# Kernel optimization log

Hardware: AMD Instinct MI355X
Metric: run time of the kernel (lower is better)

The kernel has to match this reference:

```python
import jax, jax.numpy as jnp
from jax import lax
import numpy as np

EPSILON = 22.6  # Cech radius; ~mean pairwise distance of N(0,1) points in 256-d


def _betti1(x, eps):
    """Faithful port of compute_betti_number for one epsilon. x: (B,T,C)."""
    B, T, C = x.shape
    # pairwise squared distances; compare d2 < eps^2 == (dist < eps), avoids sqrt
    sq = jnp.sum(x * x, axis=-1)                                  # (B,T)
    d2 = sq[:, :, None] + sq[:, None, :] - 2.0 * jnp.einsum('btc,bsc->bts', x, x)
    adj = d2 < (eps * eps)                                        # (B,T,T) bool; diagonal True (dist 0 < eps), matching torch
    adj = lax.stop_gradient(adj)                                  # original detaches x before topology
    # original: n_edges = np.sum(adjacency) // 2, diagonal included
    n_edges = jnp.sum(adj, axis=(1, 2)).astype(jnp.int32) // 2    # (B,)
    # connected components via min-label propagation + pointer jumping
    labels0 = jnp.broadcast_to(jnp.arange(T, dtype=jnp.int32), (B, T))

    def cond(state):
        return state[1]

    def body(state):
        labels, _ = state
        # min label among neighbors (diag True includes self)
        prop = jnp.min(jnp.where(adj, labels[:, None, :], T), axis=2).astype(jnp.int32)
        new = jnp.minimum(labels, prop)
        new = jnp.take_along_axis(new, new, axis=1)               # pointer jump -> O(log) convergence
        return new, jnp.any(new != labels)

    labels, _ = lax.while_loop(cond, body, (labels0, jnp.array(True)))
    # converged label = min index in component -> count roots
    n_comp = jnp.sum(labels == jnp.arange(T, dtype=jnp.int32)[None, :], axis=1).astype(jnp.int32)
    betti1 = jnp.maximum(0, n_edges - T + n_comp)                 # max(0, E - V + C)
    return betti1


def reference(x_before, x_after):
    betti_before = _betti1(x_before, EPSILON)
    betti_after = _betti1(x_after, EPSILON)
    diff = betti_after.astype(jnp.float32) - betti_before.astype(jnp.float32)
    return jnp.mean(diff * diff)


def setup_inputs() -> dict:
    key = jax.random.key(0)
    k1, k2 = jax.random.split(key)
    B, T, C = 4, 4096, 256
    x_before = jax.random.normal(k1, (B, T, C), dtype=jnp.float32)
    x_after = jax.random.normal(k2, (B, T, C), dtype=jnp.float32)
    return {"x_before": x_before, "x_after": x_after}
```

## Files before the change

kernel.cpp:

```cpp
#include <hip/hip_runtime.h>
#include <stdint.h>

#define TDIM 4096
#define CDIM 256
#define NMAT 8

typedef __attribute__((ext_vector_type(8))) __bf16 bf16x8;
typedef __attribute__((ext_vector_type(4))) float f32x4;

__device__ __forceinline__ unsigned short f2bf(float f) {
  unsigned int u = __float_as_uint(f);
  return (unsigned short)((u + 0x7FFFu + ((u >> 16) & 1u)) >> 16);
}
__device__ __forceinline__ void g2lds16(const void* g, void* l) {
  __builtin_amdgcn_global_load_lds((__attribute__((address_space(1))) void*)(void*)g,
                                   (__attribute__((address_space(3))) void*)l, 16, 0, 0);
}
__device__ __forceinline__ unsigned long long shfl_xor_u64(unsigned long long v, int m) {
  int lo = __shfl_xor((int)(unsigned int)(v & 0xFFFFFFFFull), m);
  int hi = __shfl_xor((int)(unsigned int)(v >> 32), m);
  return ((unsigned long long)(unsigned int)hi << 32) | (unsigned int)lo;
}

__global__ __launch_bounds__(256) void prep_kernel(
    const float* __restrict__ xb, const float* __restrict__ xa,
    unsigned short* __restrict__ xhi, float* __restrict__ sq) {
  const int wid = threadIdx.x >> 6, lane = threadIdx.x & 63;
  const int gr = blockIdx.x * 4 + wid;
  const int mb = gr >> 12;
  const size_t rowoff = (size_t)gr * CDIM;
  const float* src = (mb < 4) ? (xb + rowoff) : (xa + rowoff - (size_t)4 * TDIM * CDIM);

  float4 v = ((const float4*)src)[lane];
  float vv[4] = {v.x, v.y, v.z, v.w};
  unsigned short h[4];
  float ss = 0.f;
#pragma unroll
  for (int c = 0; c < 4; ++c) {
    h[c] = f2bf(vv[c]);
    ss += vv[c] * vv[c];
  }
  *(ushort4*)&xhi[rowoff + lane * 4] = make_ushort4(h[0], h[1], h[2], h[3]);
#pragma unroll
  for (int off = 32; off; off >>= 1) ss += __shfl_down(ss, off);
  if (lane == 0) sq[gr] = ss;
}

__global__ __launch_bounds__(256) void prep4_kernel(
    const float* __restrict__ src0, unsigned short* __restrict__ xhi,
    float* __restrict__ sq4) {
  const int wid = threadIdx.x >> 6, lane = threadIdx.x & 63;
  const int gr = blockIdx.x * 4 + wid;
  const size_t rowoff = (size_t)gr * CDIM;
  float4 v = ((const float4*)(src0 + rowoff))[lane];
  float vv[4] = {v.x, v.y, v.z, v.w};
  unsigned short h[4];
  float ss = 0.f;
#pragma unroll
  for (int c = 0; c < 4; ++c) {
    h[c] = f2bf(vv[c]);
    ss += vv[c] * vv[c];
  }
  *(ushort4*)&xhi[rowoff + lane * 4] = make_ushort4(h[0], h[1], h[2], h[3]);
#pragma unroll
  for (int off = 32; off; off >>= 1) ss += __shfl_down(ss, off);
  if (lane == 0) sq4[gr] = ss;
}

__global__ __launch_bounds__(256, 3) void gram_kernel(
    const unsigned short* __restrict__ xhi, const float* __restrict__ sq,
    unsigned long long* __restrict__ adj, int mb_base, int mbits) {
  __shared__ unsigned short As[128 * 64];
  __shared__ unsigned short Bs[128 * 64];

  const int tid = threadIdx.x;
  const int wid = tid >> 6, lane = tid & 63;
  const int wr = wid >> 1, wc = wid & 1;

  const int mbl = blockIdx.x & ((1 << mbits) - 1);
  const int mb = mb_base + mbl;
  int rem = blockIdx.x >> mbits;
  int ti = 0;
  while (rem >= 32 - ti) { rem -= 32 - ti; ++ti; }
  const int tj = ti + rem;

  const unsigned short* hi = xhi + (size_t)mbl * TDIM * CDIM;
  const float* sqm = sq + (size_t)mb * TDIM;

  f32x4 acc[4][4] = {};

  const int ldrow = (lane >> 3);
  const int ldcol = ((lane & 7) ^ ldrow) * 8;

  for (int ks = 0; ks < 4; ++ks) {
    const int kcol = ks * 64;
    __syncthreads();
#pragma unroll
    for (int i = 0; i < 4; ++i) {
      const int chunk = wid * 4 + i;
      const int row = chunk * 8 + ldrow;
      g2lds16(hi + (size_t)(ti * 128 + row) * CDIM + kcol + ldcol, &As[chunk * 512]);
      g2lds16(hi + (size_t)(tj * 128 + row) * CDIM + kcol + ldcol, &Bs[chunk * 512]);
    }
    asm volatile("s_waitcnt vmcnt(0)" ::: "memory");
    __syncthreads();
#pragma unroll
    for (int kk = 0; kk < 2; ++kk) {
      bf16x8 a[4], b[4];
      const int hi16 = lane >> 4;
#pragma unroll
      for (int m = 0; m < 4; ++m) {
        const int row = wr * 64 + m * 16 + (lane & 15);
        a[m] = *(const bf16x8*)&As[row * 64 + (((kk * 4 + hi16) ^ (row & 7)) * 8)];
      }
#pragma unroll
      for (int n = 0; n < 4; ++n) {
        const int row = wc * 64 + n * 16 + (lane & 15);
        b[n] = *(const bf16x8*)&Bs[row * 64 + (((kk * 4 + hi16) ^ (row & 7)) * 8)];
      }
#pragma unroll
      for (int m = 0; m < 4; ++m)
#pragma unroll
        for (int n = 0; n < 4; ++n)
          acc[m][n] = __builtin_amdgcn_mfma_f32_16x16x32_bf16(a[m], b[n], acc[m][n], 0, 0, 0);
    }
  }

  const float EPS2 = (float)(22.6 * 22.6);
  unsigned long long* adjm = adj + (size_t)mb * TDIM * 64;
  const int gt = (lane >> 2) & 3;
  const int mtgt = lane >> 4, rtgt = lane & 3;
  unsigned long long vrow = 0;

  float4 srv[4];
#pragma unroll
  for (int m = 0; m < 4; ++m)
    srv[m] = *(const float4*)&sqm[ti * 128 + wr * 64 + m * 16 + (lane >> 4) * 4];
  float scv[4];
#pragma unroll
  for (int n = 0; n < 4; ++n) scv[n] = sqm[tj * 128 + wc * 64 + n * 16 + (lane & 15)];

#pragma unroll
  for (int m = 0; m < 4; ++m) {
#pragma unroll
    for (int r = 0; r < 4; ++r) {
      const float srr = ((const float*)&srv[m])[r];
      unsigned long long bl[4];
#pragma unroll
      for (int n = 0; n < 4; ++n) {
        const float d2 = srr + scv[n] - 2.0f * acc[m][n][r];
        bl[n] = __ballot(d2 < EPS2);
      }
      if (m == mtgt && r == rtgt)
        vrow = ((bl[0] >> (16 * gt)) & 0xFFFFULL)         | (((bl[1] >> (16 * gt)) & 0xFFFFULL) << 16) |
               (((bl[2] >> (16 * gt)) & 0xFFFFULL) << 32) | (((bl[3] >> (16 * gt)) & 0xFFFFULL) << 48);
    }
  }
  adjm[(size_t)(ti * 128 + wr * 64 + lane) * 64 + tj * 2 + wc] = vrow;

  if (ti != tj) {
    const unsigned long long mk[6] = {
        0x5555555555555555ull, 0x3333333333333333ull, 0x0F0F0F0F0F0F0F0Full,
        0x00FF00FF00FF00FFull, 0x0000FFFF0000FFFFull, 0x00000000FFFFFFFFull};
#pragma unroll
    for (int s = 0; s < 6; ++s) {
      const int d = 1 << s;
      const unsigned long long m = mk[s];
      unsigned long long t = shfl_xor_u64(vrow, d);
      if ((lane & d) == 0) vrow = (vrow & m) | ((t & m) << d);
      else                 vrow = (vrow & ~m) | ((t & ~m) >> d);
    }
    adjm[(size_t)(tj * 128 + wc * 64 + lane) * 64 + ti * 2 + wr] = vrow;
  }
}

__global__ __launch_bounds__(256) void cc_pass1_kernel(const unsigned long long* __restrict__ adj,
                                                       int* __restrict__ gnxt,
                                                       unsigned int* __restrict__ edgepart) {
  __shared__ unsigned int wcnt[4];
  const int wid = threadIdx.x >> 6, lane = threadIdx.x & 63;
  const int grow = blockIdx.x * 4 + wid;
  unsigned long long w = adj[(size_t)grow * 64 + lane];
  int cand = w ? (lane * 64 + __ffsll(w) - 1) : 0x7fffffff;
  unsigned int c = (unsigned int)__popcll(w);
#pragma unroll
  for (int off = 32; off; off >>= 1) {
    cand = min(cand, __shfl_down(cand, off));
    c += __shfl_down(c, off);
  }
  if (lane == 0) {
    gnxt[grow] = min(cand, grow & (TDIM - 1));
    wcnt[wid] = c;
  }
  __syncthreads();
  if (threadIdx.x == 0)
    edgepart[blockIdx.x] = wcnt[0] + wcnt[1] + wcnt[2] + wcnt[3];
}

__global__ __launch_bounds__(1024) void cc_iter_kernel(const unsigned long long* __restrict__ adj,
                                                       const int* __restrict__ gnxt,
                                                       int* __restrict__ ncomp) {
  __shared__ int lab[TDIM];
  __shared__ int nxt[TDIM];
  __shared__ int changed;
  __shared__ int croots;
  const int mb = blockIdx.x;
  const unsigned long long* A = adj + (size_t)mb * TDIM * 64;
  const int tid = threadIdx.x;

  for (int i = tid; i < TDIM; i += 1024) nxt[i] = gnxt[mb * TDIM + i];
  __syncthreads();
  for (int i = tid; i < TDIM; i += 1024) lab[i] = nxt[nxt[i]];
  __syncthreads();

  for (int it = 0; it < 96; ++it) {
    if (tid == 0) changed = 0;
    __syncthreads();
    for (int i = tid; i < TDIM; i += 1024) {
      const int cur = lab[i];
      int mn = cur;
      if (cur > 0) {
        for (int wd = 0; wd < 64 && mn > 0; ++wd) {
          unsigned long long w = A[(size_t)i * 64 + wd];
          while (w && mn > 0) {
            const int bit = __ffsll(w) - 1;
            w &= w - 1;
            mn = min(mn, lab[wd * 64 + bit]);
          }
        }
        if (mn < cur) changed = 1;
      }
      nxt[i] = mn;
    }
    __syncthreads();
    const int ch = changed;
    for (int i = tid; i < TDIM; i += 1024) lab[i] = nxt[nxt[i]];
    __syncthreads();
    if (!ch) break;
  }

  if (tid == 0) croots = 0;
  __syncthreads();
  int c = 0;
  for (int i = tid; i < TDIM; i += 1024) c += (lab[i] == i);
  atomicAdd(&croots, c);
  __syncthreads();
  if (tid == 0) ncomp[mb] = croots;
}

__global__ __launch_bounds__(512) void final_kernel(const unsigned int* __restrict__ edgepart,
                                                    const int* __restrict__ ncomp,
                                                    float* __restrict__ out) {
  __shared__ unsigned long long es[8];
  const int wid = threadIdx.x >> 6, lane = threadIdx.x & 63;
  unsigned long long s = 0;
  for (int i = lane; i < 1024; i += 64) s += edgepart[wid * 1024 + i];
#pragma unroll
  for (int off = 32; off; off >>= 1) s += __shfl_down(s, off);
  if (lane == 0) es[wid] = s;
  __syncthreads();
  if (threadIdx.x == 0) {
    double acc = 0.0;
    for (int b = 0; b < 4; ++b) {
      long long e0 = (long long)(es[b] >> 1);
      long long bet0 = e0 - TDIM + (long long)ncomp[b];
      if (bet0 < 0) bet0 = 0;
      long long e1 = (long long)(es[4 + b] >> 1);
      long long bet1 = e1 - TDIM + (long long)ncomp[4 + b];
      if (bet1 < 0) bet1 = 0;
      double d = (double)(bet1 - bet0);
      acc += d * d;
    }
    out[0] = (float)(acc * 0.25);
  }
}

extern "C" void kernel_launch(void* const* d_in, const int* in_sizes, int n_in,
                              void* d_out, int out_size, void* d_ws, size_t ws_size,
                              hipStream_t stream) {
  (void)in_sizes; (void)n_in; (void)out_size;
  const float* xb = (const float*)d_in[0];
  const float* xa = (const float*)d_in[1];
  char* ws = (char*)d_ws;

  const bool big = (ws_size == 0) || (ws_size >= ((size_t)34 << 20));

  if (big) {
    const size_t XHI_OFF = 0;
    const size_t ADJ_OFF = (size_t)NMAT * TDIM * CDIM * 2;
    const size_t SQ_OFF  = ADJ_OFF + (size_t)NMAT * TDIM * 64 * 8;
    const size_t NC_OFF  = SQ_OFF + (size_t)NMAT * TDIM * 4;
    const size_t GNXT_OFF = NC_OFF + 64;
    const size_t EDGE_OFF = GNXT_OFF + (size_t)NMAT * TDIM * 4;

    unsigned short* xhi = (unsigned short*)(ws + XHI_OFF);
    unsigned long long* adj = (unsigned long long*)(ws + ADJ_OFF);
    float* sq = (float*)(ws + SQ_OFF);
    int* ncomp = (int*)(ws + NC_OFF);
    int* gnxt = (int*)(ws + GNXT_OFF);
    unsigned int* edgepart = (unsigned int*)(ws + EDGE_OFF);

    prep_kernel<<<NMAT * TDIM / 4, 256, 0, stream>>>(xb, xa, xhi, sq);
    gram_kernel<<<NMAT * 528, 256, 0, stream>>>(xhi, sq, adj, 0, 3);
    cc_pass1_kernel<<<NMAT * TDIM / 4, 256, 0, stream>>>(adj, gnxt, edgepart);
    cc_iter_kernel<<<NMAT, 1024, 0, stream>>>(adj, gnxt, ncomp);
    final_kernel<<<1, 512, 0, stream>>>(edgepart, ncomp, (float*)d_out);
  } else {
    const size_t XHI_OFF = 0;
    const size_t ADJ_OFF = (size_t)4 * TDIM * CDIM * 2;
    const size_t SQ_OFF  = ADJ_OFF + (size_t)NMAT * TDIM * 64 * 8;
    const size_t NC_OFF  = SQ_OFF + (size_t)NMAT * TDIM * 4;
    const size_t GNXT_OFF = NC_OFF + 64;
    const size_t EDGE_OFF = GNXT_OFF + (size_t)NMAT * TDIM * 4;

    unsigned short* xhi = (unsigned short*)(ws + XHI_OFF);
    unsigned long long* adj = (unsigned long long*)(ws + ADJ_OFF);
    float* sq = (float*)(ws + SQ_OFF);
    int* ncomp = (int*)(ws + NC_OFF);
    int* gnxt = (int*)(ws + GNXT_OFF);
    unsigned int* edgepart = (unsigned int*)(ws + EDGE_OFF);

    prep4_kernel<<<TDIM, 256, 0, stream>>>(xb, xhi, sq);
    gram_kernel<<<4 * 528, 256, 0, stream>>>(xhi, sq, adj, 0, 2);
    prep4_kernel<<<TDIM, 256, 0, stream>>>(xa, xhi, sq + (size_t)4 * TDIM);
    gram_kernel<<<4 * 528, 256, 0, stream>>>(xhi, sq, adj, 4, 2);
    cc_pass1_kernel<<<NMAT * TDIM / 4, 256, 0, stream>>>(adj, gnxt, edgepart);
    cc_iter_kernel<<<NMAT, 1024, 0, stream>>>(adj, gnxt, ncomp);
    final_kernel<<<1, 512, 0, stream>>>(edgepart, ncomp, (float*)d_out);
  }
}
```

Before: 85.12 us.

## Fuse edge counting and first-neighbor init into gram kernel, drop cc_pass1

Removes the cc_pass1 kernel, which re-read the full 8x4096x4096-bit adjacency to count edges and find each row's first neighbor. The gram kernel now popcounts each tile row and adds the count to a per-matrix edge sum with one atomic per wave. It also atomicMin's the first-neighbor label from the ti==0 tiles into gnxt, which the prep kernels initialize to the identity. The final kernel then reads the per-matrix sums directly instead of reducing partials, saving a full adjacency pass and a launch at the cost of atomics in the gram epilogue.

```diff
diff --git a/kernel.cpp b/kernel.cpp
--- a/kernel.cpp
+++ b/kernel.cpp
@@ -24,13 +24,16 @@
 
 __global__ __launch_bounds__(256) void prep_kernel(
     const float* __restrict__ xb, const float* __restrict__ xa,
-    unsigned short* __restrict__ xhi, float* __restrict__ sq) {
+    unsigned short* __restrict__ xhi, float* __restrict__ sq,
+    int* __restrict__ gnxt, unsigned int* __restrict__ edgesum) {
   const int wid = threadIdx.x >> 6, lane = threadIdx.x & 63;
   const int gr = blockIdx.x * 4 + wid;
   const int mb = gr >> 12;
   const size_t rowoff = (size_t)gr * CDIM;
   const float* src = (mb < 4) ? (xb + rowoff) : (xa + rowoff - (size_t)4 * TDIM * CDIM);
 
+  if (blockIdx.x == 0 && threadIdx.x < 8) edgesum[threadIdx.x] = 0u;
+
   float4 v = ((const float4*)src)[lane];
   float vv[4] = {v.x, v.y, v.z, v.w};
   unsigned short h[4];
@@ -44,14 +47,19 @@
 #pragma unroll
   for (int off = 32; off; off >>= 1) ss += __shfl_down(ss, off);
   if (lane == 0) sq[gr] = ss;
+  if (lane == 1) gnxt[gr] = gr & (TDIM - 1);
 }
 
 __global__ __launch_bounds__(256) void prep4_kernel(
     const float* __restrict__ src0, unsigned short* __restrict__ xhi,
-    float* __restrict__ sq4) {
+    float* __restrict__ sq4, int* __restrict__ gnxt4,
+    unsigned int* __restrict__ edgesum4) {
   const int wid = threadIdx.x >> 6, lane = threadIdx.x & 63;
   const int gr = blockIdx.x * 4 + wid;
   const size_t rowoff = (size_t)gr * CDIM;
+
+  if (blockIdx.x == 0 && threadIdx.x < 4) edgesum4[threadIdx.x] = 0u;
+
   float4 v = ((const float4*)(src0 + rowoff))[lane];
   float vv[4] = {v.x, v.y, v.z, v.w};
   unsigned short h[4];
@@ -65,11 +73,13 @@
 #pragma unroll
   for (int off = 32; off; off >>= 1) ss += __shfl_down(ss, off);
   if (lane == 0) sq4[gr] = ss;
+  if (lane == 1) gnxt4[gr] = gr & (TDIM - 1);
 }
 
 __global__ __launch_bounds__(256, 3) void gram_kernel(
     const unsigned short* __restrict__ xhi, const float* __restrict__ sq,
-    unsigned long long* __restrict__ adj, int mb_base, int mbits) {
+    unsigned long long* __restrict__ adj, int* __restrict__ gnxt,
+    unsigned int* __restrict__ edgesum, int mb_base, int mbits) {
   __shared__ unsigned short As[128 * 64];
   __shared__ unsigned short Bs[128 * 64];
 
@@ -158,6 +168,15 @@
   }
   adjm[(size_t)(ti * 128 + wr * 64 + lane) * 64 + tj * 2 + wc] = vrow;
 
+  {
+    unsigned int pc = (unsigned int)__popcll(vrow);
+#pragma unroll
+    for (int off = 32; off; off >>= 1) pc += __shfl_down(pc, off);
+    if (lane == 0 && pc) atomicAdd(&edgesum[mb], (ti != tj) ? pc * 2u : pc);
+  }
+  if (ti == 0 && tj == 0 && wc == 0 && vrow)
+    atomicMin(&gnxt[mb * TDIM + wr * 64 + lane], __ffsll(vrow) - 1);
+
   if (ti != tj) {
     const unsigned long long mk[6] = {
         0x5555555555555555ull, 0x3333333333333333ull, 0x0F0F0F0F0F0F0F0Full,
@@ -171,30 +190,9 @@
       else                 vrow = (vrow & ~m) | ((t & ~m) >> d);
     }
     adjm[(size_t)(tj * 128 + wc * 64 + lane) * 64 + ti * 2 + wr] = vrow;
-  }
-}
-
-__global__ __launch_bounds__(256) void cc_pass1_kernel(const unsigned long long* __restrict__ adj,
-                                                       int* __restrict__ gnxt,
-                                                       unsigned int* __restrict__ edgepart) {
-  __shared__ unsigned int wcnt[4];
-  const int wid = threadIdx.x >> 6, lane = threadIdx.x & 63;
-  const int grow = blockIdx.x * 4 + wid;
-  unsigned long long w = adj[(size_t)grow * 64 + lane];
-  int cand = w ? (lane * 64 + __ffsll(w) - 1) : 0x7fffffff;
-  unsigned int c = (unsigned int)__popcll(w);
-#pragma unroll
-  for (int off = 32; off; off >>= 1) {
-    cand = min(cand, __shfl_down(cand, off));
-    c += __shfl_down(c, off);
-  }
-  if (lane == 0) {
-    gnxt[grow] = min(cand, grow & (TDIM - 1));
-    wcnt[wid] = c;
-  }
-  __syncthreads();
-  if (threadIdx.x == 0)
-    edgepart[blockIdx.x] = wcnt[0] + wcnt[1] + wcnt[2] + wcnt[3];
+    if (ti == 0 && wr == 0 && vrow)
+      atomicMin(&gnxt[mb * TDIM + tj * 128 + wc * 64 + lane], __ffsll(vrow) - 1);
+  }
 }
 
 __global__ __launch_bounds__(1024) void cc_iter_kernel(const unsigned long long* __restrict__ adj,
@@ -248,24 +246,16 @@
   if (tid == 0) ncomp[mb] = croots;
 }
 
-__global__ __launch_bounds__(512) void final_kernel(const unsigned int* __restrict__ edgepart,
-                                                    const int* __restrict__ ncomp,
-                                                    float* __restrict__ out) {
-  __shared__ unsigned long long es[8];
-  const int wid = threadIdx.x >> 6, lane = threadIdx.x & 63;
-  unsigned long long s = 0;
-  for (int i = lane; i < 1024; i += 64) s += edgepart[wid * 1024 + i];
-#pragma unroll
-  for (int off = 32; off; off >>= 1) s += __shfl_down(s, off);
-  if (lane == 0) es[wid] = s;
-  __syncthreads();
+__global__ __launch_bounds__(64) void final_kernel(const unsigned int* __restrict__ edgesum,
+                                                   const int* __restrict__ ncomp,
+                                                   float* __restrict__ out) {
   if (threadIdx.x == 0) {
     double acc = 0.0;
     for (int b = 0; b < 4; ++b) {
-      long long e0 = (long long)(es[b] >> 1);
+      long long e0 = (long long)(edgesum[b] >> 1);
       long long bet0 = e0 - TDIM + (long long)ncomp[b];
       if (bet0 < 0) bet0 = 0;
-      long long e1 = (long long)(es[4 + b] >> 1);
+      long long e1 = (long long)(edgesum[4 + b] >> 1);
       long long bet1 = e1 - TDIM + (long long)ncomp[4 + b];
       if (bet1 < 0) bet1 = 0;
       double d = (double)(bet1 - bet0);
@@ -290,42 +280,41 @@
     const size_t ADJ_OFF = (size_t)NMAT * TDIM * CDIM * 2;
     const size_t SQ_OFF  = ADJ_OFF + (size_t)NMAT * TDIM * 64 * 8;
     const size_t NC_OFF  = SQ_OFF + (size_t)NMAT * TDIM * 4;
-    const size_t GNXT_OFF = NC_OFF + 64;
-    const size_t EDGE_OFF = GNXT_OFF + (size_t)NMAT * TDIM * 4;
+    const size_t ES_OFF  = NC_OFF + 64;
+    const size_t GNXT_OFF = ES_OFF + 64;
 
     unsigned short* xhi = (unsigned short*)(ws + XHI_OFF);
     unsigned long long* adj = (unsigned long long*)(ws + ADJ_OFF);
     float* sq = (float*)(ws + SQ_OFF);
     int* ncomp = (int*)(ws + NC_OFF);
+    unsigned int* edgesum = (unsigned int*)(ws + ES_OFF);
     int* gnxt = (int*)(ws + GNXT_OFF);
-    unsigned int* edgepart = (unsigned int*)(ws + EDGE_OFF);
-
-    prep_kernel<<<NMAT * TDIM / 4, 256, 0, stream>>>(xb, xa, xhi, sq);
-    gram_kernel<<<NMAT * 528, 256, 0, stream>>>(xhi, sq, adj, 0, 3);
-    cc_pass1_kernel<<<NMAT * TDIM / 4, 256, 0, stream>>>(adj, gnxt, edgepart);
+
+    prep_kernel<<<NMAT * TDIM / 4, 256, 0, stream>>>(xb, xa, xhi, sq, gnxt, edgesum);
+    gram_kernel<<<NMAT * 528, 256, 0, stream>>>(xhi, sq, adj, gnxt, edgesum, 0, 3);
     cc_iter_kernel<<<NMAT, 1024, 0, stream>>>(adj, gnxt, ncomp);
-    final_kernel<<<1, 512, 0, stream>>>(edgepart, ncomp, (float*)d_out);
+    final_kernel<<<1, 64, 0, stream>>>(edgesum, ncomp, (float*)d_out);
   } else {
     const size_t XHI_OFF = 0;
     const size_t ADJ_OFF = (size_t)4 * TDIM * CDIM * 2;
     const size_t SQ_OFF  = ADJ_OFF + (size_t)NMAT * TDIM * 64 * 8;
     const size_t NC_OFF  = SQ_OFF + (size_t)NMAT * TDIM * 4;
-    const size_t GNXT_OFF = NC_OFF + 64;
-    const size_t EDGE_OFF = GNXT_OFF + (size_t)NMAT * TDIM * 4;
+    const size_t ES_OFF  = NC_OFF + 64;
+    const size_t GNXT_OFF = ES_OFF + 64;
 
     unsigned short* xhi = (unsigned short*)(ws + XHI_OFF);
     unsigned long long* adj = (unsigned long long*)(ws + ADJ_OFF);
     float* sq = (float*)(ws + SQ_OFF);
     int* ncomp = (int*)(ws + NC_OFF);
+    unsigned int* edgesum = (unsigned int*)(ws + ES_OFF);
     int* gnxt = (int*)(ws + GNXT_OFF);
-    unsigned int* edgepart = (unsigned int*)(ws + EDGE_OFF);
-
-    prep4_kernel<<<TDIM, 256, 0, stream>>>(xb, xhi, sq);
-    gram_kernel<<<4 * 528, 256, 0, stream>>>(xhi, sq, adj, 0, 2);
-    prep4_kernel<<<TDIM, 256, 0, stream>>>(xa, xhi, sq + (size_t)4 * TDIM);
-    gram_kernel<<<4 * 528, 256, 0, stream>>>(xhi, sq, adj, 4, 2);
-    cc_pass1_kernel<<<NMAT * TDIM / 4, 256, 0, stream>>>(adj, gnxt, edgepart);
+
+    prep4_kernel<<<TDIM, 256, 0, stream>>>(xb, xhi, sq, gnxt, edgesum);
+    gram_kernel<<<4 * 528, 256, 0, stream>>>(xhi, sq, adj, gnxt, edgesum, 0, 2);
+    prep4_kernel<<<TDIM, 256, 0, stream>>>(xa, xhi, sq + (size_t)4 * TDIM,
+                                           gnxt + (size_t)4 * TDIM, edgesum + 4);
+    gram_kernel<<<4 * 528, 256, 0, stream>>>(xhi, sq, adj, gnxt, edgesum, 4, 2);
     cc_iter_kernel<<<NMAT, 1024, 0, stream>>>(adj, gnxt, ncomp);
-    final_kernel<<<1, 512, 0, stream>>>(edgepart, ncomp, (float*)d_out);
-  }
-}
+    final_kernel<<<1, 64, 0, stream>>>(edgesum, ncomp, (float*)d_out);
+  }
+}
```

After: 231.5 us. +171.9%, slower.
